# Kernel optimization log

Measured on AMD Instinct MI355X. Metric: run time of the kernel, lower is better.

Reference implementation:

```python
import jax, jax.numpy as jnp
import numpy as np

B, T, C, H, HD = 2, 2048, 768, 12, 64


def setup_inputs() -> dict:
    key = jax.random.key(0)
    k0, k1, k2, k3 = jax.random.split(key, 4)
    x = jax.random.normal(k0, (B, T, C), dtype=jnp.float32)
    w_attn = jax.random.normal(k1, (3 * H * HD, C), dtype=jnp.float32) * 0.02
    b_attn = jnp.zeros((3 * H * HD,), dtype=jnp.float32)
    w_proj = jax.random.normal(k2, (C, H * HD), dtype=jnp.float32) * 0.02
    b_proj = jnp.zeros((C,), dtype=jnp.float32)
    sel_w = jax.random.normal(k3, (H,), dtype=jnp.float32) * 0.3
    return {"x": x, "w_attn": w_attn, "b_attn": b_attn,
            "w_proj": w_proj, "b_proj": b_proj, "sel_w": sel_w}


def reference(x, w_attn, b_attn, w_proj, b_proj, sel_w):
    Bc, Tc, Cc = x.shape
    Hc = sel_w.shape[0]
    HDc = w_attn.shape[0] // (3 * Hc)
    qkv = x @ w_attn.T + b_attn                          # [B,T,3*H*HD]
    q, k, v = jnp.split(qkv, 3, axis=2)
    q = q.reshape(Bc, Tc, Hc, HDc).transpose(0, 2, 1, 3)  # [B,H,T,HD]
    k = k.reshape(Bc, Tc, Hc, HDc).transpose(0, 2, 1, 3)
    v = v.reshape(Bc, Tc, Hc, HDc).transpose(0, 2, 1, 3)

    scale = 1.0 / np.sqrt(HDc).astype(np.float32)
    att = jnp.einsum('bhid,bhjd->bhij', q, k) * scale    # [B,H,T,T]
    causal = jnp.tril(jnp.ones((Tc, Tc), dtype=bool))
    neg_inf = jnp.asarray(-jnp.inf, dtype=att.dtype)
    att = jnp.where(causal[None, None], att, neg_inf)

    # selection head: per-head linear combo of (causally-zeroed) logits
    att0 = jnp.where(causal[None, None], att, 0.0)       # -inf -> 0 before combo
    S = jnp.einsum('bhij,h->bij', att0, sel_w)           # [B,T,T], bias=False
    S = jnp.where(causal[None], S, 0.0)
    S = jax.nn.relu(S)
    S = S.at[..., 0].set(0.0)                            # protect_bos_token
    S = S * (1.0 - jnp.eye(Tc, dtype=S.dtype))           # prevent_from_masking_myself

    FF = jnp.cumsum(S, axis=-2)                          # forgetting accumulation over rows
    FF_shifted = jnp.concatenate(
        [jnp.zeros_like(FF[..., :1, :]), FF[..., :-1, :]], axis=-2)

    att = jax.nn.softmax(att - FF_shifted[:, None], axis=-1)
    y = jnp.einsum('bhij,bhjd->bhid', att, v)            # [B,H,T,HD]
    y = y.transpose(0, 2, 1, 3).reshape(Bc, Tc, Hc * HDc)
    return y @ w_proj.T + b_proj
```

## Files before the change

### kernel.cpp

```cpp
#include <hip/hip_runtime.h>

#define B_   2
#define T_   2048
#define C_   768
#define H_   12
#define HD_  64
#define M_   (B_ * T_)
#define N3_  (3 * C_)
#define KB_  (C_ * 2)

typedef __bf16 bf16_t;
typedef bf16_t bf16x8 __attribute__((ext_vector_type(8)));
typedef float  floatx4 __attribute__((ext_vector_type(4)));

__device__ inline floatx4 mfma_bf16(bf16x8 a, bf16x8 b, floatx4 c) {
    return __builtin_amdgcn_mfma_f32_16x16x32_bf16(a, b, c, 0, 0, 0);
}

__device__ __forceinline__ void async_copy16(const void* g, void* l) {
    __builtin_amdgcn_global_load_lds(
        (const __attribute__((address_space(1))) void*)g,
        (__attribute__((address_space(3))) void*)l, 16, 0, 0);
}

__device__ __forceinline__ bf16x8 frag_read(const char* ldsbase, int row, int quad) {
    int slot = quad ^ ((row >> 1) & 3);
    return *(const bf16x8*)(ldsbase + row * 64 + slot * 16);
}

template<bool TRIPLE>
__device__ __forceinline__ void gemm_loop8(
    const char* Ah, const char* Al, const char* Bh, const char* Bl,
    char* lds, floatx4 (&acc)[4][2])
{
    int tid = threadIdx.x, lane = tid & 63, wave = tid >> 6;
    int l15 = lane & 15, quad = lane >> 4;
    int wr = wave >> 2, wc = wave & 3;
    const int PH = TRIPLE ? 32768 : 16384;
    auto stage1 = [&](const char* tile, char* base, int k0) {
        int p = tid;
        int r = p >> 2, slot = p & 3;
        int g = slot ^ ((r >> 1) & 3);
        async_copy16(tile + (size_t)r * KB_ + k0 + g * 16, base + p * 16);
    };
    auto stage = [&](int ph, int k0) {
        char* base = lds + ph * PH;
        stage1(Ah, base, k0);
        stage1(Bh, base + 8192, k0);
        if (TRIPLE) {
            stage1(Al, base + 16384, k0);
            stage1(Bl, base + 24576, k0);
        }
    };
    stage(0, 0);
    int ph = 0;
#pragma unroll 1
    for (int k0 = 0; k0 < KB_; k0 += 64) {
        __syncthreads();
        if (k0 + 64 < KB_) stage(ph ^ 1, k0 + 64);
        char* base = lds + ph * PH;
        bf16x8 ah[4], al[4], bh[2], bl[2];
#pragma unroll
        for (int t = 0; t < 4; ++t) {
            ah[t] = frag_read(base, wr * 64 + t * 16 + l15, quad);
            if (TRIPLE)
                al[t] = frag_read(base + 16384, wr * 64 + t * 16 + l15, quad);
        }
#pragma unroll
        for (int t = 0; t < 2; ++t) {
            bh[t] = frag_read(base + 8192, wc * 32 + t * 16 + l15, quad);
            if (TRIPLE)
                bl[t] = frag_read(base + 24576, wc * 32 + t * 16 + l15, quad);
        }
#pragma unroll
        for (int mi = 0; mi < 4; ++mi)
#pragma unroll
            for (int ni = 0; ni < 2; ++ni) {
                acc[mi][ni] = mfma_bf16(ah[mi], bh[ni], acc[mi][ni]);
                if (TRIPLE) {
                    acc[mi][ni] = mfma_bf16(ah[mi], bl[ni], acc[mi][ni]);
                    acc[mi][ni] = mfma_bf16(al[mi], bh[ni], acc[mi][ni]);
                }
            }
        ph ^= 1;
    }
}

__global__ __launch_bounds__(256) void prep_kernel(
    const float* __restrict__ x, const float* __restrict__ w_attn,
    const float* __restrict__ w_proj,
    bf16_t* __restrict__ x_hi, bf16_t* __restrict__ x_lo,
    bf16_t* __restrict__ w_hi, bf16_t* __restrict__ w_lo,
    bf16_t* __restrict__ wp_b, int nx, int nw, int np)
{
    int gid = blockIdx.x * 256 + threadIdx.x;
    if (gid < nx) {
        float f = x[gid];
        bf16_t h = (bf16_t)f;
        x_hi[gid] = h;
        x_lo[gid] = (bf16_t)(f - (float)h);
    } else if (gid < nx + nw) {
        int i = gid - nx;
        float f = w_attn[i];
        bf16_t h = (bf16_t)f;
        w_hi[i] = h;
        w_lo[i] = (bf16_t)(f - (float)h);
    } else if (gid < nx + nw + np) {
        int i = gid - nx - nw;
        wp_b[i] = (bf16_t)w_proj[i];
    }
}

__global__ __launch_bounds__(512) void qkv_gemm(
    const bf16_t* __restrict__ x_hi, const bf16_t* __restrict__ x_lo,
    const bf16_t* __restrict__ w_hi, const bf16_t* __restrict__ w_lo,
    const float* __restrict__ bias, const float* __restrict__ selw,
    bf16_t* __restrict__ q_hi, bf16_t* __restrict__ q_lo,
    bf16_t* __restrict__ kw_hi, bf16_t* __restrict__ kw_lo,
    bf16_t* __restrict__ k_b, bf16_t* __restrict__ v_b)
{
    extern __shared__ char lds[];
    int m0 = blockIdx.x * 128, n0 = blockIdx.y * 128;
    floatx4 acc[4][2];
#pragma unroll
    for (int i = 0; i < 4; ++i)
#pragma unroll
        for (int j = 0; j < 2; ++j) acc[i][j] = (floatx4){0.f, 0.f, 0.f, 0.f};
    if (n0 >= 2 * C_) {
        gemm_loop8<false>((const char*)(x_hi + (size_t)m0 * C_), nullptr,
                          (const char*)(w_hi + (size_t)n0 * C_), nullptr, lds, acc);
    } else {
        gemm_loop8<true>((const char*)(x_hi + (size_t)m0 * C_),
                         (const char*)(x_lo + (size_t)m0 * C_),
                         (const char*)(w_hi + (size_t)n0 * C_),
                         (const char*)(w_lo + (size_t)n0 * C_), lds, acc);
    }

    int tid = threadIdx.x, lane = tid & 63, wave = tid >> 6;
    int l15 = lane & 15, quad = lane >> 4;
    int wr = wave >> 2, wc = wave & 3;
    int cb = n0 + wc * 32;
#pragma unroll
    for (int ni = 0; ni < 2; ++ni) {
        int col = cb + ni * 16 + l15;
        float bb = bias[col];
#pragma unroll
        for (int mi = 0; mi < 4; ++mi)
#pragma unroll
            for (int r = 0; r < 4; ++r) {
                int row = m0 + wr * 64 + mi * 16 + quad * 4 + r;
                float v = acc[mi][ni][r] + bb;
                if (cb < C_) {
                    float vs = v * 0.125f;
                    bf16_t h = (bf16_t)vs;
                    q_hi[(size_t)row * C_ + col] = h;
                    q_lo[(size_t)row * C_ + col] = (bf16_t)(vs - (float)h);
                } else if (cb < 2 * C_) {
                    int c2 = col - C_;
                    k_b[(size_t)row * C_ + c2] = (bf16_t)v;
                    float kw = v * selw[c2 >> 6];
                    bf16_t h = (bf16_t)kw;
                    kw_hi[(size_t)row * C_ + c2] = h;
                    kw_lo[(size_t)row * C_ + c2] = (bf16_t)(kw - (float)h);
                } else {
                    v_b[(size_t)row * C_ + (col - 2 * C_)] = (bf16_t)v;
                }
            }
    }
}

#define SEG_    16
#define SEGLEN_ (T_ / SEG_)

__global__ __launch_bounds__(512) void s_gemm(
    const bf16_t* __restrict__ q_hi, const bf16_t* __restrict__ q_lo,
    const bf16_t* __restrict__ kw_hi, const bf16_t* __restrict__ kw_lo,
    float* __restrict__ SF, float* __restrict__ segsum)
{
    extern __shared__ char lds[];
    int t = blockIdx.x, b = blockIdx.z;
    int it = (int)((sqrtf(8.f * t + 1.f) - 1.f) * 0.5f);
    while ((it + 1) * (it + 2) / 2 <= t) ++it;
    while (it * (it + 1) / 2 > t) --it;
    int jt = t - it * (it + 1) / 2;
    int i0 = it * 128, j0 = jt * 128;
    float* out = SF + (size_t)b * T_ * T_;

    floatx4 acc[4][2];
#pragma unroll
    for (int i = 0; i < 4; ++i)
#pragma unroll
        for (int j = 0; j < 2; ++j) acc[i][j] = (floatx4){0.f, 0.f, 0.f, 0.f};
    size_t arow = ((size_t)b * T_ + i0) * C_;
    size_t brow = ((size_t)b * T_ + j0) * C_;
    gemm_loop8<true>((const char*)(q_hi + arow), (const char*)(q_lo + arow),
                     (const char*)(kw_hi + brow), (const char*)(kw_lo + brow),
                     lds, acc);

    int tid = threadIdx.x, lane = tid & 63, wave = tid >> 6;
    int l15 = lane & 15, quad = lane >> 4;
    int wr = wave >> 2, wc = wave & 3;
    float colsum[2] = {0.f, 0.f};
#pragma unroll
    for (int ni = 0; ni < 2; ++ni) {
        int j = j0 + wc * 32 + ni * 16 + l15;
#pragma unroll
        for (int mi = 0; mi < 4; ++mi)
#pragma unroll
            for (int r = 0; r < 4; ++r) {
                int i = i0 + wr * 64 + mi * 16 + quad * 4 + r;
                float s = acc[mi][ni][r];
                s = (j >= 1 && j < i) ? fmaxf(s, 0.f) : 0.f;
                out[(size_t)i * T_ + j] = s;
                colsum[ni] += s;
            }
    }
#pragma unroll
    for (int ni = 0; ni < 2; ++ni) {
        colsum[ni] += __shfl_xor(colsum[ni], 16);
        colsum[ni] += __shfl_xor(colsum[ni], 32);
    }
    float* red = (float*)lds;
    if (quad == 0) {
#pragma unroll
        for (int ni = 0; ni < 2; ++ni)
            red[wr * 128 + wc * 32 + ni * 16 + l15] = colsum[ni];
    }
    __syncthreads();
    if (tid < 128) {
        float ssum = red[tid] + red[128 + tid];
        segsum[((size_t)b * SEG_ + it) * T_ + j0 + tid] = ssum;
    }
}

__global__ __launch_bounds__(256) void scan_apply(
    float* __restrict__ SF, const float* __restrict__ segsum)
{
    int gid  = blockIdx.x * 256 + threadIdx.x;
    int j    = gid & (T_ - 1);
    int rest = gid >> 11;
    int seg  = rest & (SEG_ - 1);
    int b    = rest >> 4;
    if (seg * SEGLEN_ + SEGLEN_ - 1 < j) return;
    float run = 0.f;
    for (int s = 0; s < seg; ++s) {
        float v = (s * SEGLEN_ + SEGLEN_ - 1 <= j) ? 0.f
                : segsum[((size_t)b * SEG_ + s) * T_ + j];
        run += v;
    }
    float* col = SF + (size_t)b * T_ * T_ + (size_t)(seg * SEGLEN_) * T_ + j;
#pragma unroll 4
    for (int i = 0; i < SEGLEN_; ++i) {
        float s = col[(size_t)i * T_];
        s = (seg * SEGLEN_ + i > j) ? s : 0.f;
        col[(size_t)i * T_] = run;
        run += s;
    }
}

__global__ __launch_bounds__(256) void vt_kernel(
    const bf16_t* __restrict__ v_b, bf16_t* __restrict__ vt)
{
    __shared__ bf16_t tile[64][72];
    int t0 = blockIdx.x * 64, h = blockIdx.y, b = blockIdx.z;
    int tid = threadIdx.x;
    int r = tid >> 2, sl = tid & 3;
    const bf16_t* src = v_b + ((size_t)(b * T_ + t0 + r)) * C_ + h * HD_ + sl * 16;
    *(int4*)&tile[r][sl * 16]     = *(const int4*)src;
    *(int4*)&tile[r][sl * 16 + 8] = *(const int4*)(src + 8);
    __syncthreads();
    int hd = tid >> 2, q = tid & 3;
#pragma unroll
    for (int half = 0; half < 2; ++half) {
        int c0 = (q * 2 + half) * 8;
        union { int4 i4; bf16_t e[8]; } u;
#pragma unroll
        for (int kk = 0; kk < 8; ++kk) u.e[kk] = tile[c0 + kk][hd];
        *(int4*)(vt + ((size_t)(b * H_ + h) * HD_ + hd) * T_ + t0 + c0) = u.i4;
    }
}

__global__ __launch_bounds__(256) void attn_kernel(
    const bf16_t* __restrict__ q_b, const bf16_t* __restrict__ k_b,
    const bf16_t* __restrict__ vt_g, const float* __restrict__ FF,
    bf16_t* __restrict__ y_b, float* __restrict__ opart,
    float* __restrict__ lpart)
{
    __shared__ __align__(16) char KL[2][8192];
    __shared__ __align__(16) char VL[2][8192];
    __shared__ __align__(16) bf16_t PB[4][1024];

    int tid = threadIdx.x, lane = tid & 63, wave = tid >> 6;
    int l15 = lane & 15, quad = lane >> 4;
    int u = blockIdx.x & 15, g = blockIdx.x >> 4;
    int tile, jlo, jhi, half;
    bool split;
    if (g == 0)      { tile = 16 + u; jlo = 0;  jhi = 15;       half = 0; split = true;  }
    else if (g == 1) { tile = u;      jlo = 0;  jhi = u;        half = 0; split = false; }
    else             { tile = 31 - u; jlo = 16; jhi = 31 - u;   half = 1; split = true;  }
    int h = blockIdx.y, b = blockIdx.z;
    int i0w = tile * 64 + wave * 16;
    const floatx4 fzero = {0.f, 0.f, 0.f, 0.f};

    const bf16_t* qrow = q_b + ((size_t)b * T_ + i0w + l15) * C_ + h * HD_;
    bf16x8 qa0 = *(const bf16x8*)(qrow + quad * 8);
    bf16x8 qa1 = *(const bf16x8*)(qrow + 32 + quad * 8);

    const bf16_t* kbase = k_b + (size_t)b * T_ * C_ + h * HD_;
    const bf16_t* vbase = vt_g + (size_t)(b * H_ + h) * HD_ * T_;
    const float* fpr[4];
#pragma unroll
    for (int r = 0; r < 4; ++r)
        fpr[r] = FF + ((size_t)b * T_ + i0w + quad * 4 + r) * T_ + jlo * 64 + l15;

    auto stage = [&](int ph, int j0) {
#pragma unroll
        for (int i = 0; i < 2; ++i) {
            int p = (wave * 2 + i) * 64 + lane;
            int r = p >> 3, sp = p & 7, s = sp ^ (r & 7);
            async_copy16(kbase + (size_t)(j0 + r) * C_ + s * 8, &KL[ph][p * 16]);
        }
#pragma unroll
        for (int i = 0; i < 2; ++i) {
            int p = (wave * 2 + i) * 64 + lane;
            int r = p >> 3, sp = p & 7, s = sp ^ (r & 7);
            async_copy16(vbase + (size_t)r * T_ + j0 + s * 8, &VL[ph][p * 16]);
        }
    };

    float l_lane[4] = {0.f, 0.f, 0.f, 0.f};
    floatx4 O[4];
#pragma unroll
    for (int nt = 0; nt < 4; ++nt) O[nt] = fzero;

    stage(0, jlo * 64);
    int ph = 0;
#pragma unroll 1
    for (int jc = jlo; jc <= jhi; ++jc) {
        __syncthreads();
        if (jc < jhi) stage(ph ^ 1, (jc + 1) * 64);

        float ff[4][4];
#pragma unroll
        for (int r = 0; r < 4; ++r) {
#pragma unroll
            for (int s = 0; s < 4; ++s) ff[s][r] = fpr[r][s * 16];
            fpr[r] += 64;
        }
        floatx4 pc[4];
#pragma unroll
        for (int s = 0; s < 4; ++s) {
            int r = s * 16 + l15;
            bf16x8 k0 = *(const bf16x8*)&KL[ph][r * 128 + ((quad     ^ (r & 7)) * 16)];
            bf16x8 k1 = *(const bf16x8*)&KL[ph][r * 128 + (((quad+4) ^ (r & 7)) * 16)];
            floatx4 p = mfma_bf16(qa0, k0, fzero);
            pc[s] = mfma_bf16(qa1, k1, p);
        }
        bool diag = (jc * 64 + 63 > i0w);
        float p[4][4];
#pragma unroll
        for (int s = 0; s < 4; ++s)
#pragma unroll
            for (int r = 0; r < 4; ++r) {
                float lg = pc[s][r] - ff[s][r] - 20.f;
                if (diag) {
                    int i = i0w + quad * 4 + r;
                    int j = jc * 64 + s * 16 + l15;
                    lg = (j <= i) ? lg : -__builtin_inff();
                }
                p[s][r] = __expf(lg);
            }
#pragma unroll
        for (int r = 0; r < 4; ++r)
            l_lane[r] += (p[0][r] + p[1][r]) + (p[2][r] + p[3][r]);

        bf16_t* Pw = &PB[wave][0];
#pragma unroll
        for (int s = 0; s < 4; ++s)
#pragma unroll
            for (int r = 0; r < 4; ++r) {
                int rr = quad * 4 + r;
                int ch = (s * 2 + (l15 >> 3)) ^ (rr & 7);
                Pw[rr * 64 + ch * 8 + (l15 & 7)] = (bf16_t)p[s][r];
            }
        asm volatile("s_waitcnt lgkmcnt(0)" ::: "memory");
        int xk = l15 & 7;
        bf16x8 pa0 = *(const bf16x8*)&Pw[l15 * 64 + ((quad ^ xk) * 8)];
        bf16x8 pa1 = *(const bf16x8*)&Pw[l15 * 64 + (((4 + quad) ^ xk) * 8)];
#pragma unroll
        for (int nt = 0; nt < 4; ++nt) {
            int r = nt * 16 + l15;
            bf16x8 v0 = *(const bf16x8*)&VL[ph][r * 128 + ((quad     ^ (r & 7)) * 16)];
            bf16x8 v1 = *(const bf16x8*)&VL[ph][r * 128 + (((quad+4) ^ (r & 7)) * 16)];
            O[nt] = mfma_bf16(pa0, v0, O[nt]);
            O[nt] = mfma_bf16(pa1, v1, O[nt]);
        }
        ph ^= 1;
    }

#pragma unroll
    for (int r = 0; r < 4; ++r)
#pragma unroll
        for (int d = 1; d < 16; d <<= 1)
            l_lane[r] += __shfl_xor(l_lane[r], d);

    if (!split) {
#pragma unroll
        for (int r = 0; r < 4; ++r) {
            float inv = 1.f / l_lane[r];
            int i = i0w + quad * 4 + r;
#pragma unroll
            for (int nt = 0; nt < 4; ++nt)
                y_b[((size_t)b * T_ + i) * C_ + h * HD_ + nt * 16 + l15] =
                    (bf16_t)(O[nt][r] * inv);
        }
    } else {
        size_t ob = ((((size_t)(b * H_ + h) * 16 + (tile - 16)) * 2 + half) * 4096);
#pragma unroll
        for (int r = 0; r < 4; ++r) {
            int rl = wave * 16 + quad * 4 + r;
#pragma unroll
            for (int nt = 0; nt < 4; ++nt)
                opart[ob + (size_t)rl * 64 + nt * 16 + l15] = O[nt][r];
        }
        if (l15 == 0) {
            size_t lb = (((size_t)(b * H_ + h) * 16 + (tile - 16)) * 2 + half) * 64;
#pragma unroll
            for (int r = 0; r < 4; ++r)
                lpart[lb + wave * 16 + quad * 4 + r] = l_lane[r];
        }
    }
}

__global__ __launch_bounds__(256) void merge_kernel(
    const float* __restrict__ opart, const float* __restrict__ lpart,
    bf16_t* __restrict__ y_b)
{
    int tt = blockIdx.x, h = blockIdx.y, b = blockIdx.z;
    size_t b0 = (((size_t)(b * H_ + h) * 16 + tt) * 2) * 4096;
    size_t l0 = (((size_t)(b * H_ + h) * 16 + tt) * 2) * 64;
    int tile = 16 + tt;
#pragma unroll 4
    for (int e = threadIdx.x; e < 4096; e += 256) {
        int row = e >> 6, col = e & 63;
        float l = lpart[l0 + row] + lpart[l0 + 64 + row];
        float o = opart[b0 + e] + opart[b0 + 4096 + e];
        y_b[((size_t)b * T_ + tile * 64 + row) * C_ + h * HD_ + col] =
            (bf16_t)(o / l);
    }
}

__global__ __launch_bounds__(512) void proj_gemm(
    const bf16_t* __restrict__ y_b, const bf16_t* __restrict__ wp_b,
    const float* __restrict__ bias, float* __restrict__ out)
{
    extern __shared__ char lds[];
    int m0 = blockIdx.x * 128, n0 = blockIdx.y * 128;
    floatx4 acc[4][2];
#pragma unroll
    for (int i = 0; i < 4; ++i)
#pragma unroll
        for (int j = 0; j < 2; ++j) acc[i][j] = (floatx4){0.f, 0.f, 0.f, 0.f};
    gemm_loop8<false>((const char*)(y_b + (size_t)m0 * C_), nullptr,
                      (const char*)(wp_b + (size_t)n0 * C_), nullptr, lds, acc);

    int tid = threadIdx.x, lane = tid & 63, wave = tid >> 6;
    int l15 = lane & 15, quad = lane >> 4;
    int wr = wave >> 2, wc = wave & 3;
#pragma unroll
    for (int ni = 0; ni < 2; ++ni) {
        int col = n0 + wc * 32 + ni * 16 + l15;
        float bb = bias[col];
#pragma unroll
        for (int mi = 0; mi < 4; ++mi)
#pragma unroll
            for (int r = 0; r < 4; ++r)
                out[(size_t)(m0 + wr * 64 + mi * 16 + quad * 4 + r) * C_ + col] =
                    acc[mi][ni][r] + bb;
    }
}

extern "C" void kernel_launch(void* const* d_in, const int* in_sizes, int n_in,
                              void* d_out, int out_size, void* d_ws, size_t ws_size,
                              hipStream_t stream)
{
    const float* x      = (const float*)d_in[0];
    const float* w_attn = (const float*)d_in[1];
    const float* b_attn = (const float*)d_in[2];
    const float* w_proj = (const float*)d_in[3];
    const float* b_proj = (const float*)d_in[4];
    const float* sel_w  = (const float*)d_in[5];
    float* out = (float*)d_out;

    char* ws = (char*)d_ws;
    size_t off = 0;
    auto alloc = [&](size_t bytes) {
        void* p = ws + off;
        off += (bytes + 255) & ~(size_t)255;
        return p;
    };
    const size_t MC2 = (size_t)M_ * C_ * 2;
    bf16_t* q_hi   = (bf16_t*)alloc(MC2);
    bf16_t* kw_hi  = (bf16_t*)alloc(MC2);
    bf16_t* k_b    = (bf16_t*)alloc(MC2);
    bf16_t* y_b    = (bf16_t*)alloc(MC2);
    bf16_t* wp_b   = (bf16_t*)alloc((size_t)C_ * C_ * 2);
    float*  segsum = (float*)alloc((size_t)B_ * SEG_ * T_ * 4);
    char* dead_base = (char*)alloc(3 * MC2);
    bf16_t* q_lo  = (bf16_t*)dead_base;
    bf16_t* kw_lo = (bf16_t*)(dead_base + MC2);
    bf16_t* v_b   = (bf16_t*)(dead_base + 2 * MC2);
    float*  opart = (float*)dead_base;
    float*  lpart = (float*)(dead_base + (size_t)B_ * H_ * 16 * 2 * 4096 * 4);
    char* shared_base = (char*)alloc((size_t)B_ * T_ * T_ * 4);
    bf16_t* x_hi = (bf16_t*)shared_base;
    bf16_t* x_lo = (bf16_t*)(shared_base + MC2);
    bf16_t* w_hi = (bf16_t*)(shared_base + 2 * MC2);
    bf16_t* w_lo = (bf16_t*)(shared_base + 2 * MC2 + (size_t)N3_ * C_ * 2);
    float*  SF   = (float*)shared_base;
    bf16_t* vt   = kw_hi;

    int nx = M_ * C_, nw = N3_ * C_, np = C_ * C_;
    int ntot = nx + nw + np;
    prep_kernel<<<dim3((ntot + 255) / 256), 256, 0, stream>>>(
        x, w_attn, w_proj, x_hi, x_lo, w_hi, w_lo, wp_b, nx, nw, np);

    qkv_gemm<<<dim3(M_ / 128, N3_ / 128), 512, 65536, stream>>>(
        x_hi, x_lo, w_hi, w_lo, b_attn, sel_w,
        q_hi, q_lo, kw_hi, kw_lo, k_b, v_b);
    s_gemm<<<dim3(136, 1, B_), 512, 65536, stream>>>(
        q_hi, q_lo, kw_hi, kw_lo, SF, segsum);
    vt_kernel<<<dim3(T_ / 64, H_, B_), 256, 0, stream>>>(v_b, vt);
    scan_apply<<<dim3(B_ * SEG_ * T_ / 256), 256, 0, stream>>>(SF, segsum);
    attn_kernel<<<dim3(48, H_, B_), 256, 0, stream>>>(
        q_hi, k_b, vt, SF, y_b, opart, lpart);
    merge_kernel<<<dim3(16, H_, B_), 256, 0, stream>>>(opart, lpart, y_b);
    proj_gemm<<<dim3(M_ / 128, C_ / 128), 512, 32768, stream>>>(y_b, wp_b, b_proj, out);
}
```

Measured before the change: 254.9 us.

## Pair causal attention tiles per block and prefetch FF values one chunk ahead

```diff
diff --git a/kernel.cpp b/kernel.cpp
--- a/kernel.cpp
+++ b/kernel.cpp
@@ -292,26 +292,13 @@
 
     int tid = threadIdx.x, lane = tid & 63, wave = tid >> 6;
     int l15 = lane & 15, quad = lane >> 4;
-    int u = blockIdx.x & 15, g = blockIdx.x >> 4;
-    int tile, jlo, jhi, half;
-    bool split;
-    if (g == 0)      { tile = 16 + u; jlo = 0;  jhi = 15;       half = 0; split = true;  }
-    else if (g == 1) { tile = u;      jlo = 0;  jhi = u;        half = 0; split = false; }
-    else             { tile = 31 - u; jlo = 16; jhi = 31 - u;   half = 1; split = true;  }
+    int u = blockIdx.x & 15;
+    int dual = blockIdx.x >> 4;
     int h = blockIdx.y, b = blockIdx.z;
-    int i0w = tile * 64 + wave * 16;
     const floatx4 fzero = {0.f, 0.f, 0.f, 0.f};
-
-    const bf16_t* qrow = q_b + ((size_t)b * T_ + i0w + l15) * C_ + h * HD_;
-    bf16x8 qa0 = *(const bf16x8*)(qrow + quad * 8);
-    bf16x8 qa1 = *(const bf16x8*)(qrow + 32 + quad * 8);
 
     const bf16_t* kbase = k_b + (size_t)b * T_ * C_ + h * HD_;
     const bf16_t* vbase = vt_g + (size_t)(b * H_ + h) * HD_ * T_;
-    const float* fpr[4];
-#pragma unroll
-    for (int r = 0; r < 4; ++r)
-        fpr[r] = FF + ((size_t)b * T_ + i0w + quad * 4 + r) * T_ + jlo * 64 + l15;
 
     auto stage = [&](int ph, int j0) {
 #pragma unroll
@@ -328,18 +315,31 @@
         }
     };
 
-    float l_lane[4] = {0.f, 0.f, 0.f, 0.f};
-    floatx4 O[4];
-#pragma unroll
-    for (int nt = 0; nt < 4; ++nt) O[nt] = fzero;
-
-    stage(0, jlo * 64);
-    int ph = 0;
+    int njobs = 1 + dual;
 #pragma unroll 1
-    for (int jc = jlo; jc <= jhi; ++jc) {
-        __syncthreads();
-        if (jc < jhi) stage(ph ^ 1, (jc + 1) * 64);
-
+    for (int job = 0; job < njobs; ++job) {
+        int tile, jlo, jhi, half, split;
+        if (!dual)         { tile = 16 + u; jlo = 0;  jhi = 15;     half = 0; split = 1; }
+        else if (job == 0) { tile = u;      jlo = 0;  jhi = u;      half = 0; split = 0; }
+        else               { tile = 31 - u; jlo = 16; jhi = 31 - u; half = 1; split = 1; }
+        int i0w = tile * 64 + wave * 16;
+
+        const bf16_t* qrow = q_b + ((size_t)b * T_ + i0w + l15) * C_ + h * HD_;
+        bf16x8 qa0 = *(const bf16x8*)(qrow + quad * 8);
+        bf16x8 qa1 = *(const bf16x8*)(qrow + 32 + quad * 8);
+
+        const float* fpr[4];
+#pragma unroll
+        for (int r = 0; r < 4; ++r)
+            fpr[r] = FF + ((size_t)b * T_ + i0w + quad * 4 + r) * T_ + jlo * 64 + l15;
+
+        float l_lane[4] = {0.f, 0.f, 0.f, 0.f};
+        floatx4 O[4];
+#pragma unroll
+        for (int nt = 0; nt < 4; ++nt) O[nt] = fzero;
+
+        if (job) __syncthreads();
+        stage(0, jlo * 64);
         float ff[4][4];
 #pragma unroll
         for (int r = 0; r < 4; ++r) {
@@ -347,87 +347,108 @@
             for (int s = 0; s < 4; ++s) ff[s][r] = fpr[r][s * 16];
             fpr[r] += 64;
         }
-        floatx4 pc[4];
-#pragma unroll
-        for (int s = 0; s < 4; ++s) {
-            int r = s * 16 + l15;
-            bf16x8 k0 = *(const bf16x8*)&KL[ph][r * 128 + ((quad     ^ (r & 7)) * 16)];
-            bf16x8 k1 = *(const bf16x8*)&KL[ph][r * 128 + (((quad+4) ^ (r & 7)) * 16)];
-            floatx4 p = mfma_bf16(qa0, k0, fzero);
-            pc[s] = mfma_bf16(qa1, k1, p);
-        }
-        bool diag = (jc * 64 + 63 > i0w);
-        float p[4][4];
-#pragma unroll
-        for (int s = 0; s < 4; ++s)
+        int ph = 0;
+#pragma unroll 1
+        for (int jc = jlo; jc <= jhi; ++jc) {
+            __syncthreads();
+            float ffn[4][4];
+            if (jc < jhi) {
+                stage(ph ^ 1, (jc + 1) * 64);
+#pragma unroll
+                for (int r = 0; r < 4; ++r) {
+#pragma unroll
+                    for (int s = 0; s < 4; ++s) ffn[s][r] = fpr[r][s * 16];
+                    fpr[r] += 64;
+                }
+            }
+            floatx4 pc[4];
+#pragma unroll
+            for (int s = 0; s < 4; ++s) {
+                int r = s * 16 + l15;
+                bf16x8 k0 = *(const bf16x8*)&KL[ph][r * 128 + ((quad     ^ (r & 7)) * 16)];
+                bf16x8 k1 = *(const bf16x8*)&KL[ph][r * 128 + (((quad+4) ^ (r & 7)) * 16)];
+                floatx4 p = mfma_bf16(qa0, k0, fzero);
+                pc[s] = mfma_bf16(qa1, k1, p);
+            }
+            bool diag = (jc * 64 + 63 > i0w);
+            float p[4][4];
+#pragma unroll
+            for (int s = 0; s < 4; ++s)
+#pragma unroll
+                for (int r = 0; r < 4; ++r) {
+                    float lg = pc[s][r] - ff[s][r] - 20.f;
+                    if (diag) {
+                        int i = i0w + quad * 4 + r;
+                        int j = jc * 64 + s * 16 + l15;
+                        lg = (j <= i) ? lg : -__builtin_inff();
+                    }
+                    p[s][r] = __expf(lg);
+                }
+#pragma unroll
+            for (int r = 0; r < 4; ++r)
+                l_lane[r] += (p[0][r] + p[1][r]) + (p[2][r] + p[3][r]);
+
+            bf16_t* Pw = &PB[wave][0];
+#pragma unroll
+            for (int s = 0; s < 4; ++s)
+#pragma unroll
+                for (int r = 0; r < 4; ++r) {
+                    int rr = quad * 4 + r;
+                    int ch = (s * 2 + (l15 >> 3)) ^ (rr & 7);
+                    Pw[rr * 64 + ch * 8 + (l15 & 7)] = (bf16_t)p[s][r];
+                }
+            asm volatile("s_waitcnt lgkmcnt(0)" ::: "memory");
+            int xk = l15 & 7;
+            bf16x8 pa0 = *(const bf16x8*)&Pw[l15 * 64 + ((quad ^ xk) * 8)];
+            bf16x8 pa1 = *(const bf16x8*)&Pw[l15 * 64 + (((4 + quad) ^ xk) * 8)];
+#pragma unroll
+            for (int nt = 0; nt < 4; ++nt) {
+                int r = nt * 16 + l15;
+                bf16x8 v0 = *(const bf16x8*)&VL[ph][r * 128 + ((quad     ^ (r & 7)) * 16)];
+                bf16x8 v1 = *(const bf16x8*)&VL[ph][r * 128 + (((quad+4) ^ (r & 7)) * 16)];
+                O[nt] = mfma_bf16(pa0, v0, O[nt]);
+                O[nt] = mfma_bf16(pa1, v1, O[nt]);
+            }
+            if (jc < jhi) {
+#pragma unroll
+                for (int s = 0; s < 4; ++s)
+#pragma unroll
+                    for (int r = 0; r < 4; ++r) ff[s][r] = ffn[s][r];
+            }
+            ph ^= 1;
+        }
+
+#pragma unroll
+        for (int r = 0; r < 4; ++r)
+#pragma unroll
+            for (int d = 1; d < 16; d <<= 1)
+                l_lane[r] += __shfl_xor(l_lane[r], d);
+
+        if (!split) {
 #pragma unroll
             for (int r = 0; r < 4; ++r) {
-                float lg = pc[s][r] - ff[s][r] - 20.f;
-                if (diag) {
-                    int i = i0w + quad * 4 + r;
-                    int j = jc * 64 + s * 16 + l15;
-                    lg = (j <= i) ? lg : -__builtin_inff();
-                }
-                p[s][r] = __expf(lg);
-            }
-#pragma unroll
-        for (int r = 0; r < 4; ++r)
-            l_lane[r] += (p[0][r] + p[1][r]) + (p[2][r] + p[3][r]);
-
-        bf16_t* Pw = &PB[wave][0];
-#pragma unroll
-        for (int s = 0; s < 4; ++s)
+                float inv = 1.f / l_lane[r];
+                int i = i0w + quad * 4 + r;
+#pragma unroll
+                for (int nt = 0; nt < 4; ++nt)
+                    y_b[((size_t)b * T_ + i) * C_ + h * HD_ + nt * 16 + l15] =
+                        (bf16_t)(O[nt][r] * inv);
+            }
+        } else {
+            size_t ob = ((((size_t)(b * H_ + h) * 16 + (tile - 16)) * 2 + half) * 4096);
 #pragma unroll
             for (int r = 0; r < 4; ++r) {
-                int rr = quad * 4 + r;
-                int ch = (s * 2 + (l15 >> 3)) ^ (rr & 7);
-                Pw[rr * 64 + ch * 8 + (l15 & 7)] = (bf16_t)p[s][r];
-            }
-        asm volatile("s_waitcnt lgkmcnt(0)" ::: "memory");
-        int xk = l15 & 7;
-        bf16x8 pa0 = *(const bf16x8*)&Pw[l15 * 64 + ((quad ^ xk) * 8)];
-        bf16x8 pa1 = *(const bf16x8*)&Pw[l15 * 64 + (((4 + quad) ^ xk) * 8)];
-#pragma unroll
-        for (int nt = 0; nt < 4; ++nt) {
-            int r = nt * 16 + l15;
-            bf16x8 v0 = *(const bf16x8*)&VL[ph][r * 128 + ((quad     ^ (r & 7)) * 16)];
-            bf16x8 v1 = *(const bf16x8*)&VL[ph][r * 128 + (((quad+4) ^ (r & 7)) * 16)];
-            O[nt] = mfma_bf16(pa0, v0, O[nt]);
-            O[nt] = mfma_bf16(pa1, v1, O[nt]);
-        }
-        ph ^= 1;
-    }
-
-#pragma unroll
-    for (int r = 0; r < 4; ++r)
-#pragma unroll
-        for (int d = 1; d < 16; d <<= 1)
-            l_lane[r] += __shfl_xor(l_lane[r], d);
-
-    if (!split) {
-#pragma unroll
-        for (int r = 0; r < 4; ++r) {
-            float inv = 1.f / l_lane[r];
-            int i = i0w + quad * 4 + r;
-#pragma unroll
-            for (int nt = 0; nt < 4; ++nt)
-                y_b[((size_t)b * T_ + i) * C_ + h * HD_ + nt * 16 + l15] =
-                    (bf16_t)(O[nt][r] * inv);
-        }
-    } else {
-        size_t ob = ((((size_t)(b * H_ + h) * 16 + (tile - 16)) * 2 + half) * 4096);
-#pragma unroll
-        for (int r = 0; r < 4; ++r) {
-            int rl = wave * 16 + quad * 4 + r;
-#pragma unroll
-            for (int nt = 0; nt < 4; ++nt)
-                opart[ob + (size_t)rl * 64 + nt * 16 + l15] = O[nt][r];
-        }
-        if (l15 == 0) {
-            size_t lb = (((size_t)(b * H_ + h) * 16 + (tile - 16)) * 2 + half) * 64;
-#pragma unroll
-            for (int r = 0; r < 4; ++r)
-                lpart[lb + wave * 16 + quad * 4 + r] = l_lane[r];
+                int rl = wave * 16 + quad * 4 + r;
+#pragma unroll
+                for (int nt = 0; nt < 4; ++nt)
+                    opart[ob + (size_t)rl * 64 + nt * 16 + l15] = O[nt][r];
+            }
+            if (l15 == 0) {
+                size_t lb = (((size_t)(b * H_ + h) * 16 + (tile - 16)) * 2 + half) * 64;
+#pragma unroll
+                for (int r = 0; r < 4; ++r)
+                    lpart[lb + wave * 16 + quad * 4 + r] = l_lane[r];
+            }
         }
     }
 }
@@ -532,7 +553,7 @@
         q_hi, q_lo, kw_hi, kw_lo, SF, segsum);
     vt_kernel<<<dim3(T_ / 64, H_, B_), 256, 0, stream>>>(v_b, vt);
     scan_apply<<<dim3(B_ * SEG_ * T_ / 256), 256, 0, stream>>>(SF, segsum);
-    attn_kernel<<<dim3(48, H_, B_), 256, 0, stream>>>(
+    attn_kernel<<<dim3(32, H_, B_), 256, 0, stream>>>(
         q_hi, k_b, vt, SF, y_b, opart, lpart);
     merge_kernel<<<dim3(16, H_, B_), 256, 0, stream>>>(opart, lpart, y_b);
     proj_gemm<<<dim3(M_ / 128, C_ / 128), 512, 32768, stream>>>(y_b, wp_b, b_proj, out);
```

After: 258.7 us. No clear change (+1.5%).

## Widen attention key/value chunk from 64 to 128 columns per iteration

Applied to the files above, without the earlier changes.

```diff
diff --git a/kernel.cpp b/kernel.cpp
--- a/kernel.cpp
+++ b/kernel.cpp
@@ -286,18 +286,19 @@
     bf16_t* __restrict__ y_b, float* __restrict__ opart,
     float* __restrict__ lpart)
 {
-    __shared__ __align__(16) char KL[2][8192];
-    __shared__ __align__(16) char VL[2][8192];
-    __shared__ __align__(16) bf16_t PB[4][1024];
+    extern __shared__ __align__(16) char lds[];
+    char* KL = lds;
+    char* VL = lds + 32768;
+    bf16_t* PBall = (bf16_t*)(lds + 65536);
 
     int tid = threadIdx.x, lane = tid & 63, wave = tid >> 6;
     int l15 = lane & 15, quad = lane >> 4;
     int u = blockIdx.x & 15, g = blockIdx.x >> 4;
     int tile, jlo, jhi, half;
     bool split;
-    if (g == 0)      { tile = 16 + u; jlo = 0;  jhi = 15;       half = 0; split = true;  }
-    else if (g == 1) { tile = u;      jlo = 0;  jhi = u;        half = 0; split = false; }
-    else             { tile = 31 - u; jlo = 16; jhi = 31 - u;   half = 1; split = true;  }
+    if (g == 0)      { tile = 16 + u; jlo = 0; jhi = 7;                   half = 0; split = true;  }
+    else if (g == 1) { tile = u;      jlo = 0; jhi = ((u + 2) >> 1) - 1;  half = 0; split = false; }
+    else             { tile = 31 - u; jlo = 8; jhi = ((33 - u) >> 1) - 1; half = 1; split = true;  }
     int h = blockIdx.y, b = blockIdx.z;
     int i0w = tile * 64 + wave * 16;
     const floatx4 fzero = {0.f, 0.f, 0.f, 0.f};
@@ -311,20 +312,23 @@
     const float* fpr[4];
 #pragma unroll
     for (int r = 0; r < 4; ++r)
-        fpr[r] = FF + ((size_t)b * T_ + i0w + quad * 4 + r) * T_ + jlo * 64 + l15;
+        fpr[r] = FF + ((size_t)b * T_ + i0w + quad * 4 + r) * T_ + jlo * 128 + l15;
 
     auto stage = [&](int ph, int j0) {
 #pragma unroll
-        for (int i = 0; i < 2; ++i) {
-            int p = (wave * 2 + i) * 64 + lane;
+        for (int i = 0; i < 4; ++i) {
+            int p = (wave * 4 + i) * 64 + lane;
             int r = p >> 3, sp = p & 7, s = sp ^ (r & 7);
-            async_copy16(kbase + (size_t)(j0 + r) * C_ + s * 8, &KL[ph][p * 16]);
-        }
-#pragma unroll
-        for (int i = 0; i < 2; ++i) {
-            int p = (wave * 2 + i) * 64 + lane;
-            int r = p >> 3, sp = p & 7, s = sp ^ (r & 7);
-            async_copy16(vbase + (size_t)r * T_ + j0 + s * 8, &VL[ph][p * 16]);
+            async_copy16(kbase + (size_t)(j0 + r) * C_ + s * 8,
+                         KL + ph * 16384 + p * 16);
+        }
+#pragma unroll
+        for (int i = 0; i < 4; ++i) {
+            int p = (wave * 4 + i) * 64 + lane;
+            int r = p >> 4, sp = p & 15;
+            int s = (sp & 8) | ((sp & 7) ^ (r & 7));
+            async_copy16(vbase + (size_t)r * T_ + j0 + s * 8,
+                         VL + ph * 16384 + p * 16);
         }
     };
 
@@ -333,67 +337,79 @@
 #pragma unroll
     for (int nt = 0; nt < 4; ++nt) O[nt] = fzero;
 
-    stage(0, jlo * 64);
+    stage(0, jlo * 128);
     int ph = 0;
 #pragma unroll 1
     for (int jc = jlo; jc <= jhi; ++jc) {
         __syncthreads();
-        if (jc < jhi) stage(ph ^ 1, (jc + 1) * 64);
-
-        float ff[4][4];
+        if (jc < jhi) stage(ph ^ 1, (jc + 1) * 128);
+
+        float ff[8][4];
 #pragma unroll
         for (int r = 0; r < 4; ++r) {
 #pragma unroll
-            for (int s = 0; s < 4; ++s) ff[s][r] = fpr[r][s * 16];
-            fpr[r] += 64;
-        }
-        floatx4 pc[4];
-#pragma unroll
-        for (int s = 0; s < 4; ++s) {
+            for (int s = 0; s < 8; ++s) ff[s][r] = fpr[r][s * 16];
+            fpr[r] += 128;
+        }
+        const char* KLp = KL + ph * 16384;
+        floatx4 pc[8];
+#pragma unroll
+        for (int s = 0; s < 8; ++s) {
             int r = s * 16 + l15;
-            bf16x8 k0 = *(const bf16x8*)&KL[ph][r * 128 + ((quad     ^ (r & 7)) * 16)];
-            bf16x8 k1 = *(const bf16x8*)&KL[ph][r * 128 + (((quad+4) ^ (r & 7)) * 16)];
+            bf16x8 k0 = *(const bf16x8*)&KLp[r * 128 + ((quad     ^ (r & 7)) * 16)];
+            bf16x8 k1 = *(const bf16x8*)&KLp[r * 128 + (((quad+4) ^ (r & 7)) * 16)];
             floatx4 p = mfma_bf16(qa0, k0, fzero);
             pc[s] = mfma_bf16(qa1, k1, p);
         }
-        bool diag = (jc * 64 + 63 > i0w);
-        float p[4][4];
-#pragma unroll
-        for (int s = 0; s < 4; ++s)
+        bool diag = (jc * 128 + 127 > i0w);
+        float p[8][4];
+#pragma unroll
+        for (int s = 0; s < 8; ++s)
 #pragma unroll
             for (int r = 0; r < 4; ++r) {
                 float lg = pc[s][r] - ff[s][r] - 20.f;
                 if (diag) {
                     int i = i0w + quad * 4 + r;
-                    int j = jc * 64 + s * 16 + l15;
+                    int j = jc * 128 + s * 16 + l15;
                     lg = (j <= i) ? lg : -__builtin_inff();
                 }
                 p[s][r] = __expf(lg);
             }
 #pragma unroll
         for (int r = 0; r < 4; ++r)
-            l_lane[r] += (p[0][r] + p[1][r]) + (p[2][r] + p[3][r]);
-
-        bf16_t* Pw = &PB[wave][0];
-#pragma unroll
-        for (int s = 0; s < 4; ++s)
+            l_lane[r] += ((p[0][r] + p[1][r]) + (p[2][r] + p[3][r]))
+                       + ((p[4][r] + p[5][r]) + (p[6][r] + p[7][r]));
+
+        bf16_t* Pw = PBall + wave * 2048;
+#pragma unroll
+        for (int s = 0; s < 8; ++s)
 #pragma unroll
             for (int r = 0; r < 4; ++r) {
                 int rr = quad * 4 + r;
-                int ch = (s * 2 + (l15 >> 3)) ^ (rr & 7);
-                Pw[rr * 64 + ch * 8 + (l15 & 7)] = (bf16_t)p[s][r];
+                int c  = s * 2 + (l15 >> 3);
+                int ch = (c & 8) | ((c & 7) ^ (rr & 7));
+                Pw[rr * 128 + ch * 8 + (l15 & 7)] = (bf16_t)p[s][r];
             }
         asm volatile("s_waitcnt lgkmcnt(0)" ::: "memory");
         int xk = l15 & 7;
-        bf16x8 pa0 = *(const bf16x8*)&Pw[l15 * 64 + ((quad ^ xk) * 8)];
-        bf16x8 pa1 = *(const bf16x8*)&Pw[l15 * 64 + (((4 + quad) ^ xk) * 8)];
+        bf16x8 pa[4];
+#pragma unroll
+        for (int gk = 0; gk < 4; ++gk) {
+            int c  = gk * 4 + quad;
+            int ch = (c & 8) | ((c & 7) ^ xk);
+            pa[gk] = *(const bf16x8*)&Pw[l15 * 128 + ch * 8];
+        }
+        const char* VLp = VL + ph * 16384;
 #pragma unroll
         for (int nt = 0; nt < 4; ++nt) {
-            int r = nt * 16 + l15;
-            bf16x8 v0 = *(const bf16x8*)&VL[ph][r * 128 + ((quad     ^ (r & 7)) * 16)];
-            bf16x8 v1 = *(const bf16x8*)&VL[ph][r * 128 + (((quad+4) ^ (r & 7)) * 16)];
-            O[nt] = mfma_bf16(pa0, v0, O[nt]);
-            O[nt] = mfma_bf16(pa1, v1, O[nt]);
+            int rv = nt * 16 + l15;
+#pragma unroll
+            for (int gk = 0; gk < 4; ++gk) {
+                int c  = gk * 4 + quad;
+                int ch = (c & 8) | ((c & 7) ^ (rv & 7));
+                bf16x8 v = *(const bf16x8*)&VLp[rv * 256 + ch * 16];
+                O[nt] = mfma_bf16(pa[gk], v, O[nt]);
+            }
         }
         ph ^= 1;
     }
@@ -532,7 +548,7 @@
         q_hi, q_lo, kw_hi, kw_lo, SF, segsum);
     vt_kernel<<<dim3(T_ / 64, H_, B_), 256, 0, stream>>>(v_b, vt);
     scan_apply<<<dim3(B_ * SEG_ * T_ / 256), 256, 0, stream>>>(SF, segsum);
-    attn_kernel<<<dim3(48, H_, B_), 256, 0, stream>>>(
+    attn_kernel<<<dim3(48, H_, B_), 256, 81920, stream>>>(
         q_hi, k_b, vt, SF, y_b, opart, lpart);
     merge_kernel<<<dim3(16, H_, B_), 256, 0, stream>>>(opart, lpart, y_b);
     proj_gemm<<<dim3(M_ / 128, C_ / 128), 512, 32768, stream>>>(y_b, wp_b, b_proj, out);
```

Measured after the change: 252.2 us. About the same (-1.0%).

## Store selection/forget matrix transposed so scan runs along contiguous rows

Applied to the files above, without the earlier changes.

```diff
diff --git a/kernel.cpp b/kernel.cpp
--- a/kernel.cpp
+++ b/kernel.cpp
@@ -12,6 +12,7 @@
 typedef __bf16 bf16_t;
 typedef bf16_t bf16x8 __attribute__((ext_vector_type(8)));
 typedef float  floatx4 __attribute__((ext_vector_type(4)));
+typedef unsigned long long u64_t;
 
 __device__ inline floatx4 mfma_bf16(bf16x8 a, bf16x8 b, floatx4 c) {
     return __builtin_amdgcn_mfma_f32_16x16x32_bf16(a, b, c, 0, 0, 0);
@@ -193,42 +194,51 @@
         for (int j = 0; j < 2; ++j) acc[i][j] = (floatx4){0.f, 0.f, 0.f, 0.f};
     size_t arow = ((size_t)b * T_ + i0) * C_;
     size_t brow = ((size_t)b * T_ + j0) * C_;
-    gemm_loop8<true>((const char*)(q_hi + arow), (const char*)(q_lo + arow),
-                     (const char*)(kw_hi + brow), (const char*)(kw_lo + brow),
+    gemm_loop8<true>((const char*)(kw_hi + brow), (const char*)(kw_lo + brow),
+                     (const char*)(q_hi + arow), (const char*)(q_lo + arow),
                      lds, acc);
 
     int tid = threadIdx.x, lane = tid & 63, wave = tid >> 6;
     int l15 = lane & 15, quad = lane >> 4;
     int wr = wave >> 2, wc = wave & 3;
-    float colsum[2] = {0.f, 0.f};
+    float rs[4][4];
+#pragma unroll
+    for (int mi = 0; mi < 4; ++mi)
+#pragma unroll
+        for (int r = 0; r < 4; ++r) rs[mi][r] = 0.f;
 #pragma unroll
     for (int ni = 0; ni < 2; ++ni) {
-        int j = j0 + wc * 32 + ni * 16 + l15;
+        int i = i0 + wc * 32 + ni * 16 + l15;
 #pragma unroll
         for (int mi = 0; mi < 4; ++mi)
 #pragma unroll
             for (int r = 0; r < 4; ++r) {
-                int i = i0 + wr * 64 + mi * 16 + quad * 4 + r;
+                int j = j0 + wr * 64 + mi * 16 + quad * 4 + r;
                 float s = acc[mi][ni][r];
                 s = (j >= 1 && j < i) ? fmaxf(s, 0.f) : 0.f;
-                out[(size_t)i * T_ + j] = s;
-                colsum[ni] += s;
+                out[(size_t)j * T_ + i] = s;
+                rs[mi][r] += s;
             }
     }
 #pragma unroll
-    for (int ni = 0; ni < 2; ++ni) {
-        colsum[ni] += __shfl_xor(colsum[ni], 16);
-        colsum[ni] += __shfl_xor(colsum[ni], 32);
-    }
+    for (int mi = 0; mi < 4; ++mi)
+#pragma unroll
+        for (int r = 0; r < 4; ++r) {
+#pragma unroll
+            for (int d = 1; d < 16; d <<= 1)
+                rs[mi][r] += __shfl_xor(rs[mi][r], d);
+        }
     float* red = (float*)lds;
-    if (quad == 0) {
-#pragma unroll
-        for (int ni = 0; ni < 2; ++ni)
-            red[wr * 128 + wc * 32 + ni * 16 + l15] = colsum[ni];
+    if (l15 == 0) {
+#pragma unroll
+        for (int mi = 0; mi < 4; ++mi)
+#pragma unroll
+            for (int r = 0; r < 4; ++r)
+                red[wc * 128 + wr * 64 + mi * 16 + quad * 4 + r] = rs[mi][r];
     }
     __syncthreads();
     if (tid < 128) {
-        float ssum = red[tid] + red[128 + tid];
+        float ssum = red[tid] + red[128 + tid] + red[256 + tid] + red[384 + tid];
         segsum[((size_t)b * SEG_ + it) * T_ + j0 + tid] = ssum;
     }
 }
@@ -248,12 +258,12 @@
                 : segsum[((size_t)b * SEG_ + s) * T_ + j];
         run += v;
     }
-    float* col = SF + (size_t)b * T_ * T_ + (size_t)(seg * SEGLEN_) * T_ + j;
+    float* col = SF + (size_t)b * T_ * T_ + (size_t)j * T_ + seg * SEGLEN_;
 #pragma unroll 4
     for (int i = 0; i < SEGLEN_; ++i) {
-        float s = col[(size_t)i * T_];
+        float s = col[i];
         s = (seg * SEGLEN_ + i > j) ? s : 0.f;
-        col[(size_t)i * T_] = run;
+        col[i] = run;
         run += s;
     }
 }
@@ -286,9 +296,10 @@
     bf16_t* __restrict__ y_b, float* __restrict__ opart,
     float* __restrict__ lpart)
 {
-    __shared__ __align__(16) char KL[2][8192];
-    __shared__ __align__(16) char VL[2][8192];
-    __shared__ __align__(16) bf16_t PB[4][1024];
+    extern __shared__ __align__(16) char lds[];
+    char* KL = lds;
+    char* VL = lds + 16384;
+    char* PB = lds + 32768;
 
     int tid = threadIdx.x, lane = tid & 63, wave = tid >> 6;
     int l15 = lane & 15, quad = lane >> 4;
@@ -311,24 +322,24 @@
     const float* fpr[4];
 #pragma unroll
     for (int r = 0; r < 4; ++r)
-        fpr[r] = FF + ((size_t)b * T_ + i0w + quad * 4 + r) * T_ + jlo * 64 + l15;
+        fpr[r] = FF + ((size_t)b * T_ + jlo * 64 + quad * 4 + r) * T_ + i0w + l15;
 
     auto stage = [&](int ph, int j0) {
 #pragma unroll
         for (int i = 0; i < 2; ++i) {
             int p = (wave * 2 + i) * 64 + lane;
             int r = p >> 3, sp = p & 7, s = sp ^ (r & 7);
-            async_copy16(kbase + (size_t)(j0 + r) * C_ + s * 8, &KL[ph][p * 16]);
+            async_copy16(kbase + (size_t)(j0 + r) * C_ + s * 8, KL + ph * 8192 + p * 16);
         }
 #pragma unroll
         for (int i = 0; i < 2; ++i) {
             int p = (wave * 2 + i) * 64 + lane;
             int r = p >> 3, sp = p & 7, s = sp ^ (r & 7);
-            async_copy16(vbase + (size_t)r * T_ + j0 + s * 8, &VL[ph][p * 16]);
+            async_copy16(vbase + (size_t)r * T_ + j0 + s * 8, VL + ph * 8192 + p * 16);
         }
     };
 
-    float l_lane[4] = {0.f, 0.f, 0.f, 0.f};
+    float l_lane = 0.f;
     floatx4 O[4];
 #pragma unroll
     for (int nt = 0; nt < 4; ++nt) O[nt] = fzero;
@@ -344,17 +355,18 @@
 #pragma unroll
         for (int r = 0; r < 4; ++r) {
 #pragma unroll
-            for (int s = 0; s < 4; ++s) ff[s][r] = fpr[r][s * 16];
-            fpr[r] += 64;
-        }
+            for (int s = 0; s < 4; ++s) ff[s][r] = fpr[r][(size_t)s * 16 * T_];
+            fpr[r] += (size_t)64 * T_;
+        }
+        const char* KLp = KL + ph * 8192;
         floatx4 pc[4];
 #pragma unroll
         for (int s = 0; s < 4; ++s) {
             int r = s * 16 + l15;
-            bf16x8 k0 = *(const bf16x8*)&KL[ph][r * 128 + ((quad     ^ (r & 7)) * 16)];
-            bf16x8 k1 = *(const bf16x8*)&KL[ph][r * 128 + (((quad+4) ^ (r & 7)) * 16)];
-            floatx4 p = mfma_bf16(qa0, k0, fzero);
-            pc[s] = mfma_bf16(qa1, k1, p);
+            bf16x8 k0 = *(const bf16x8*)&KLp[r * 128 + ((quad     ^ (r & 7)) * 16)];
+            bf16x8 k1 = *(const bf16x8*)&KLp[r * 128 + (((quad+4) ^ (r & 7)) * 16)];
+            floatx4 p = mfma_bf16(k0, qa0, fzero);
+            pc[s] = mfma_bf16(k1, qa1, p);
         }
         bool diag = (jc * 64 + 63 > i0w);
         float p[4][4];
@@ -364,50 +376,57 @@
             for (int r = 0; r < 4; ++r) {
                 float lg = pc[s][r] - ff[s][r] - 20.f;
                 if (diag) {
-                    int i = i0w + quad * 4 + r;
-                    int j = jc * 64 + s * 16 + l15;
+                    int i = i0w + l15;
+                    int j = jc * 64 + s * 16 + quad * 4 + r;
                     lg = (j <= i) ? lg : -__builtin_inff();
                 }
                 p[s][r] = __expf(lg);
             }
 #pragma unroll
-        for (int r = 0; r < 4; ++r)
-            l_lane[r] += (p[0][r] + p[1][r]) + (p[2][r] + p[3][r]);
-
-        bf16_t* Pw = &PB[wave][0];
-#pragma unroll
         for (int s = 0; s < 4; ++s)
-#pragma unroll
-            for (int r = 0; r < 4; ++r) {
-                int rr = quad * 4 + r;
-                int ch = (s * 2 + (l15 >> 3)) ^ (rr & 7);
-                Pw[rr * 64 + ch * 8 + (l15 & 7)] = (bf16_t)p[s][r];
-            }
+            l_lane += (p[s][0] + p[s][1]) + (p[s][2] + p[s][3]);
+
+        char* Pw = PB + wave * 2176;
+        int x = l15 & 7;
+#pragma unroll
+        for (int s = 0; s < 4; ++s) {
+            union { bf16_t e[4]; u64_t v; } u4;
+#pragma unroll
+            for (int r = 0; r < 4; ++r) u4.e[r] = (bf16_t)p[s][r];
+            int slot = (s * 4 + quad) ^ x;
+            *(u64_t*)(Pw + l15 * 136 + slot * 8) = u4.v;
+        }
         asm volatile("s_waitcnt lgkmcnt(0)" ::: "memory");
-        int xk = l15 & 7;
-        bf16x8 pa0 = *(const bf16x8*)&Pw[l15 * 64 + ((quad ^ xk) * 8)];
-        bf16x8 pa1 = *(const bf16x8*)&Pw[l15 * 64 + (((4 + quad) ^ xk) * 8)];
+        bf16x8 pa0, pa1;
+        {
+            union { u64_t d[2]; bf16x8 f; } c0, c1;
+            c0.d[0] = *(const u64_t*)(Pw + l15 * 136 + (((2 * quad)     ^ x) * 8));
+            c0.d[1] = *(const u64_t*)(Pw + l15 * 136 + (((2 * quad + 1) ^ x) * 8));
+            c1.d[0] = *(const u64_t*)(Pw + l15 * 136 + (((8 + 2 * quad)     ^ x) * 8));
+            c1.d[1] = *(const u64_t*)(Pw + l15 * 136 + (((8 + 2 * quad + 1) ^ x) * 8));
+            pa0 = c0.f;
+            pa1 = c1.f;
+        }
+        const char* VLp = VL + ph * 8192;
 #pragma unroll
         for (int nt = 0; nt < 4; ++nt) {
-            int r = nt * 16 + l15;
-            bf16x8 v0 = *(const bf16x8*)&VL[ph][r * 128 + ((quad     ^ (r & 7)) * 16)];
-            bf16x8 v1 = *(const bf16x8*)&VL[ph][r * 128 + (((quad+4) ^ (r & 7)) * 16)];
+            int rv = nt * 16 + l15;
+            bf16x8 v0 = *(const bf16x8*)&VLp[rv * 128 + ((quad     ^ (rv & 7)) * 16)];
+            bf16x8 v1 = *(const bf16x8*)&VLp[rv * 128 + (((quad+4) ^ (rv & 7)) * 16)];
             O[nt] = mfma_bf16(pa0, v0, O[nt]);
             O[nt] = mfma_bf16(pa1, v1, O[nt]);
         }
         ph ^= 1;
     }
 
-#pragma unroll
-    for (int r = 0; r < 4; ++r)
-#pragma unroll
-        for (int d = 1; d < 16; d <<= 1)
-            l_lane[r] += __shfl_xor(l_lane[r], d);
+    l_lane += __shfl_xor(l_lane, 16);
+    l_lane += __shfl_xor(l_lane, 32);
 
     if (!split) {
 #pragma unroll
         for (int r = 0; r < 4; ++r) {
-            float inv = 1.f / l_lane[r];
+            float lv = __shfl(l_lane, quad * 4 + r);
+            float inv = 1.f / lv;
             int i = i0w + quad * 4 + r;
 #pragma unroll
             for (int nt = 0; nt < 4; ++nt)
@@ -423,11 +442,9 @@
             for (int nt = 0; nt < 4; ++nt)
                 opart[ob + (size_t)rl * 64 + nt * 16 + l15] = O[nt][r];
         }
-        if (l15 == 0) {
+        if (quad == 0) {
             size_t lb = (((size_t)(b * H_ + h) * 16 + (tile - 16)) * 2 + half) * 64;
-#pragma unroll
-            for (int r = 0; r < 4; ++r)
-                lpart[lb + wave * 16 + quad * 4 + r] = l_lane[r];
+            lpart[lb + wave * 16 + l15] = l_lane;
         }
     }
 }
@@ -532,7 +549,7 @@
         q_hi, q_lo, kw_hi, kw_lo, SF, segsum);
     vt_kernel<<<dim3(T_ / 64, H_, B_), 256, 0, stream>>>(v_b, vt);
     scan_apply<<<dim3(B_ * SEG_ * T_ / 256), 256, 0, stream>>>(SF, segsum);
-    attn_kernel<<<dim3(48, H_, B_), 256, 0, stream>>>(
+    attn_kernel<<<dim3(48, H_, B_), 256, 41472, stream>>>(
         q_hi, k_b, vt, SF, y_b, opart, lpart);
     merge_kernel<<<dim3(16, H_, B_), 256, 0, stream>>>(opart, lpart, y_b);
     proj_gemm<<<dim3(M_ / 128, C_ / 128), 512, 32768, stream>>>(y_b, wp_b, b_proj, out);
```

Measured after the change: 260.3 us. +2.1%, slower.
